# Performance work log

Measured on AMD Instinct MI355X. Metric: run time of the kernel, lower is better.

Reference implementation:

```python
import jax, jax.numpy as jnp
import numpy as np

B, C, H, W = 64, 512, 8, 8
K = 100            # num_class
H1, HID, L = 64, 128, 32   # ae_hidden[0], fixed hidd, ae_latent
CLIP = 100.0       # CSSRClassifier.clip_len
RED = -0.1         # model='pcssr' -> -1, times gamma=0.1
PUSH_THRESH = 10000.0


def setup_inputs() -> dict:
    key = jax.random.key(0)
    ks = jax.random.split(key, 9)
    s = lambda fan_in: 1.0 / np.sqrt(fan_in)  # kaiming-ish 1x1 conv init scale
    return {
        "x": jax.random.normal(ks[0], (B, C, H, W), jnp.float32),
        "ycls": jax.random.randint(ks[1], (B,), 0, K),
        "safe_margin_all": jax.random.normal(ks[2], (K,), jnp.float32),
        "safe_distance_all": jax.random.normal(ks[3], (K,), jnp.float32),
        "W1": jax.random.normal(ks[4], (K, H1, C), jnp.float32) * s(C),
        "W2": jax.random.normal(ks[5], (K, HID, H1), jnp.float32) * s(H1),
        "W3": jax.random.normal(ks[6], (K, L, HID), jnp.float32) * s(HID),
        "prototypes": jax.random.normal(ks[7], (K, L, H, W), jnp.float32),
        "prototypes1": jax.random.normal(ks[8], (K, L, H, W), jnp.float32),
    }


def reference(x, ycls, safe_margin_all, safe_distance_all, W1, W2, W3, prototypes, prototypes1):
    P = H * W
    xf = x.reshape(B, C, P)
    # per-class 1x1-conv encoder (tanh after every conv), batched over classes k
    h = jnp.tanh(jnp.einsum('koc,bcp->kbop', W1, xf))      # [K,B,H1,P]
    h = jnp.tanh(jnp.einsum('koi,kbip->kbop', W2, h))      # [K,B,HID,P]
    lt = jnp.tanh(jnp.einsum('koi,kbip->kbop', W3, h))     # [K,B,L,P]
    p = prototypes.reshape(K, 1, L, P)
    p1 = prototypes1.reshape(K, 1, L, P)
    # squared-L2 distance over channel dim, scaled by reduction, clipped
    er = jnp.clip(jnp.sum((lt - p) ** 2, axis=2) * RED, -CLIP, CLIP)    # [K,B,P]
    er1 = jnp.clip(jnp.sum((lt - p1) ** 2, axis=2) * RED, -CLIP, CLIP)  # [K,B,P]
    # training losses (pull on er1, push on er), vectorized across classes
    f = jnp.sum(er, axis=2)    # [K,B] spatial-summed errors
    f1 = jnp.sum(er1, axis=2)  # [K,B]
    cls_ids = jnp.arange(K)[:, None]
    mask_eq = (ycls[None, :] == cls_ids).astype(f.dtype)   # [K,B]
    n_eq = jnp.sum(mask_eq, axis=1)
    pull = jnp.sum(jnp.where(n_eq > 0,
                             jnp.sum(f1 * mask_eq, axis=1) / jnp.maximum(n_eq, 1.0),
                             0.0))
    comb = (1.0 - mask_eq) * (f < PUSH_THRESH).astype(f.dtype)
    n_comb = jnp.sum(comb, axis=1)
    push = jnp.sum(jnp.where(n_comb > 0,
                             jnp.sum(f * comb, axis=1) / jnp.maximum(n_comb, 1.0),
                             0.0))
    # cat per-class [B,1,H,W] errors along dim 1 -> [B,K,H,W]
    logits = jnp.transpose(er, (1, 0, 2)).reshape(B, K, H, W)
    logits1 = jnp.transpose(er1, (1, 0, 2)).reshape(B, K, H, W)
    return logits, logits1, pull, push
```

## Files before the change

kernel.cpp:

```cpp
#include <hip/hip_runtime.h>

typedef short  s16x8  __attribute__((ext_vector_type(8)));
typedef float  f32x16 __attribute__((ext_vector_type(16)));
typedef unsigned short u16;
typedef unsigned int   u32;
typedef unsigned long long u64b;

#define MFMA32(a,b,c) __builtin_amdgcn_mfma_f32_32x32x16_bf16((a),(b),(c),0,0,0)
#define KCLS 100
#define VMCNT(n) asm volatile("s_waitcnt vmcnt(" #n ")" ::: "memory")
#define BAR()    __builtin_amdgcn_s_barrier()

__device__ __forceinline__ u16 f2bf(float f) {
  return (u16)(__builtin_bit_cast(unsigned, f) >> 16);
}

__device__ __forceinline__ u32 pk2bf(float lo, float hi) {
#if __has_builtin(__builtin_amdgcn_perm)
  return __builtin_amdgcn_perm(__builtin_bit_cast(u32, hi),
                               __builtin_bit_cast(u32, lo), 0x07060302u);
#else
  return (__builtin_bit_cast(u32, lo) >> 16) | (__builtin_bit_cast(u32, hi) & 0xffff0000u);
#endif
}

__device__ __forceinline__ float tanh_fast(float x) {
  float e = __builtin_amdgcn_exp2f(x * 2.8853900817779268f);
  return 1.0f - 2.0f * __builtin_amdgcn_rcpf(e + 1.0f);
}

__device__ __forceinline__ void ld_lds16(const void* g, void* l) {
  __builtin_amdgcn_global_load_lds(
      (const __attribute__((address_space(1))) unsigned char*)g,
      (__attribute__((address_space(3))) unsigned char*)l, 16, 0, 0);
}

__global__ void prep(const float* __restrict__ x, const float* __restrict__ w1,
                     const float* __restrict__ w2, const float* __restrict__ w3,
                     u16* __restrict__ xF, u16* __restrict__ W1F,
                     u16* __restrict__ W2F, u16* __restrict__ W3F,
                     float* __restrict__ fz, float* __restrict__ out2) {
  __shared__ float tile[64][65];
  const int bid = blockIdx.x, t = threadIdx.x;
  if (bid == 0 && t < 2) out2[t] = 0.f;
  if (bid < 512) {
    const int b = bid >> 3, ck = bid & 7;
    #pragma unroll
    for (int j = 0; j < 4; j++) {
      int e4 = j * 1024 + t * 4;
      int c = e4 >> 6, p0 = e4 & 63;
      float4 v = *(const float4*)(x + ((size_t)b * 512 + ck * 64 + c) * 64 + p0);
      tile[c][p0] = v.x; tile[c][p0 + 1] = v.y; tile[c][p0 + 2] = v.z; tile[c][p0 + 3] = v.w;
    }
    __syncthreads();
    #pragma unroll
    for (int i = 0; i < 2; i++) {
      int s = i * 256 + t;
      int ksl = s >> 7, ph = (s >> 6) & 1, lane = s & 63;
      int cb = ksl * 16 + (lane >> 5) * 8, pp = ph * 32 + (lane & 31);
      u16 o[8];
      #pragma unroll
      for (int jj = 0; jj < 8; jj++) o[jj] = f2bf(tile[cb + jj][pp]);
      *(uint4*)(xF + (((size_t)b * 64 + (ck * 4 + ksl) * 2 + ph) * 512) + lane * 8) = *(uint4*)o;
    }
  } else if (bid < 1312) {
    const int wb = bid - 512, k = wb >> 3, ct = wb & 7;
    #pragma unroll
    for (int j = 0; j < 4; j++) {
      int e4 = j * 1024 + t * 4;
      int r = e4 >> 6, c = e4 & 63;
      float4 v = *(const float4*)(w1 + ((size_t)k * 64 + r) * 512 + ct * 64 + c);
      tile[r][c] = v.x; tile[r][c + 1] = v.y; tile[r][c + 2] = v.z; tile[r][c + 3] = v.w;
    }
    __syncthreads();
    #pragma unroll
    for (int i = 0; i < 2; i++) {
      int s = i * 256 + t;
      int frl = s >> 6, lane = s & 63;
      int m = (frl & 1) * 32 + (lane & 31);
      int cl = (frl >> 1) * 16 + (lane >> 5) * 8;
      u16 o[8];
      #pragma unroll
      for (int jj = 0; jj < 8; jj++) o[jj] = f2bf(tile[m][cl + jj]);
      *(uint4*)(W1F + ((size_t)(k * 64 + ct * 8 + frl) * 512) + lane * 8) = *(uint4*)o;
    }
  } else if (bid < 1512) {
    const int wb = bid - 1312, k = wb >> 1, mt = wb & 1;
    #pragma unroll
    for (int j = 0; j < 4; j++) {
      int e4 = j * 1024 + t * 4;
      int r = e4 >> 6, c = e4 & 63;
      float4 v = *(const float4*)(w2 + ((size_t)k * 128 + mt * 64 + r) * 64 + c);
      tile[r][c] = v.x; tile[r][c + 1] = v.y; tile[r][c + 2] = v.z; tile[r][c + 3] = v.w;
    }
    __syncthreads();
    #pragma unroll
    for (int i = 0; i < 2; i++) {
      int s = i * 256 + t;
      int frl = s >> 6, lane = s & 63;
      int kb = frl >> 1, m4l = frl & 1;
      int ml = m4l * 32 + (lane & 31);
      int cl = kb * 16 + (lane >> 5) * 8;
      u16 o[8];
      #pragma unroll
      for (int jj = 0; jj < 8; jj++) o[jj] = f2bf(tile[ml][cl + jj]);
      *(uint4*)(W2F + ((size_t)(k * 16 + kb * 4 + mt * 2 + m4l) * 512) + lane * 8) = *(uint4*)o;
    }
  } else if (bid < 1612) {
    const int k = bid - 1512;
    #pragma unroll
    for (int j = 0; j < 4; j++) {
      int e4 = j * 1024 + t * 4;
      int r = e4 >> 7, c = e4 & 127;
      float4 v = *(const float4*)(w3 + ((size_t)k * 32 + r) * 128 + c);
      int rr = r + ((c >> 6) << 5), cc = c & 63;
      tile[rr][cc] = v.x; tile[rr][cc + 1] = v.y; tile[rr][cc + 2] = v.z; tile[rr][cc + 3] = v.w;
    }
    __syncthreads();
    #pragma unroll
    for (int i = 0; i < 2; i++) {
      int s = i * 256 + t;
      int frl = s >> 6, lane = s & 63;
      int m = lane & 31;
      int c0 = frl * 16 + (lane >> 5) * 8;
      int rr = m + ((c0 >> 6) << 5), cc = c0 & 63;
      u16 o[8];
      #pragma unroll
      for (int jj = 0; jj < 8; jj++) o[jj] = f2bf(tile[rr][cc + jj]);
      *(uint4*)(W3F + ((size_t)(k * 8 + frl) * 512) + lane * 8) = *(uint4*)o;
    }
  } else {
    int i4 = (bid - 1612) * 256 + t;
    if (i4 < 3200) {
      float4 z = {0.f, 0.f, 0.f, 0.f};
      *(float4*)(fz + (size_t)i4 * 4) = z;
    }
  }
}

template<int GG>
__device__ __forceinline__ s16x8 mk_bfrag(const f32x16 a) {
  u32 P0 = pk2bf(tanh_fast(a[8 * GG + 0]), tanh_fast(a[8 * GG + 1]));
  u32 P1 = pk2bf(tanh_fast(a[8 * GG + 2]), tanh_fast(a[8 * GG + 3]));
  u32 Q0 = pk2bf(tanh_fast(a[8 * GG + 4]), tanh_fast(a[8 * GG + 5]));
  u32 Q1 = pk2bf(tanh_fast(a[8 * GG + 6]), tanh_fast(a[8 * GG + 7]));
  asm("v_permlane32_swap_b32 %0, %1" : "+v"(P0), "+v"(Q0));
  asm("v_permlane32_swap_b32 %0, %1" : "+v"(P1), "+v"(Q1));
  int4 wv = { (int)P0, (int)P1, (int)Q0, (int)Q1 };
  return __builtin_bit_cast(s16x8, wv);
}

__global__ __launch_bounds__(256, 4) void cssr_main(
    const u16* __restrict__ W1F, const u16* __restrict__ W2F, const u16* __restrict__ W3F,
    const u16* __restrict__ xF, const float* __restrict__ protos,
    const float* __restrict__ protos1, float* __restrict__ out,
    float* __restrict__ fw, float* __restrict__ f1w)
{
  __shared__ u16 pool[20480];
  const int bid = blockIdx.x;
  const int k = bid >> 5, bpair = bid & 31;
  const int tid = threadIdx.x, w = tid >> 6, lane = tid & 63;
  const int bq = w >> 1, ph = w & 1;
  const int b = bpair * 2 + bq;
  const int h = lane >> 5, nn = lane & 31;

  const u16* xw  = xF  + ((size_t)b * 64) * 512 + lane * 8;
  const u16* w1w = W1F + ((size_t)k * 64) * 512 + lane * 8;

  s16x8 Bc[4], Bn[4];
  #pragma unroll
  for (int ksl = 0; ksl < 4; ksl++)
    Bc[ksl] = *(const s16x8*)(xw + (ksl * 2 + ph) * 512);
  ld_lds16(w1w + (w * 2 + 0) * 512, &pool[(2 * w + 0) * 512]);
  ld_lds16(w1w + (w * 2 + 1) * 512, &pool[(2 * w + 1) * 512]);

  f32x16 acc1[2] = {};
  #pragma unroll
  for (int ci = 0; ci < 8; ci++) {
    const int cb = ci & 1;
    if (ci < 7) {
      #pragma unroll
      for (int ksl = 0; ksl < 4; ksl++)
        Bn[ksl] = *(const s16x8*)(xw + (((ci + 1) * 4 + ksl) * 2 + ph) * 512);
      ld_lds16(w1w + (((ci + 1) * 4 + w) * 2 + 0) * 512, &pool[(cb ^ 1) * 4096 + (2 * w + 0) * 512]);
      ld_lds16(w1w + (((ci + 1) * 4 + w) * 2 + 1) * 512, &pool[(cb ^ 1) * 4096 + (2 * w + 1) * 512]);
    } else {
      #pragma unroll
      for (int j = 0; j < 4; j++)
        ld_lds16(W2F + ((size_t)k * 16 + w * 4 + j) * 512 + lane * 8,
                 &pool[8192 + (w * 4 + j) * 512]);
      ld_lds16(W3F + ((size_t)k * 8 + w * 2 + 0) * 512 + lane * 8, &pool[16384 + (w * 2 + 0) * 512]);
      ld_lds16(W3F + ((size_t)k * 8 + w * 2 + 1) * 512 + lane * 8, &pool[16384 + (w * 2 + 1) * 512]);
    }
    VMCNT(6); BAR();
    __builtin_amdgcn_s_setprio(1);
    #pragma unroll
    for (int ksl = 0; ksl < 4; ksl++) {
      s16x8 A0 = *(const s16x8*)&pool[cb * 4096 + (ksl * 2 + 0) * 512 + lane * 8];
      s16x8 A1 = *(const s16x8*)&pool[cb * 4096 + (ksl * 2 + 1) * 512 + lane * 8];
      acc1[0] = MFMA32(A0, Bc[ksl], acc1[0]);
      acc1[1] = MFMA32(A1, Bc[ksl], acc1[1]);
    }
    __builtin_amdgcn_s_setprio(0);
    if (ci < 7) {
      #pragma unroll
      for (int ksl = 0; ksl < 4; ksl++) Bc[ksl] = Bn[ksl];
      BAR();
    }
  }

  s16x8 b1[4];
  b1[0] = mk_bfrag<0>(acc1[0]); b1[1] = mk_bfrag<1>(acc1[0]);
  b1[2] = mk_bfrag<0>(acc1[1]); b1[3] = mk_bfrag<1>(acc1[1]);

  VMCNT(2); BAR();

  f32x16 acc2[4] = {};
  __builtin_amdgcn_s_setprio(1);
  #pragma unroll
  for (int kb = 0; kb < 4; kb++) {
    #pragma unroll
    for (int m4 = 0; m4 < 4; m4++) {
      s16x8 A = *(const s16x8*)&pool[8192 + (kb * 4 + m4) * 512 + lane * 8];
      acc2[m4] = MFMA32(A, b1[kb], acc2[m4]);
    }
  }
  __builtin_amdgcn_s_setprio(0);

  VMCNT(0); BAR();

  const int p = ph * 32 + nn;
  const float* pr  = protos  + (size_t)k * 2048 + p;
  const float* pr1 = protos1 + (size_t)k * 2048 + p;
  float prv[16], pr1v[16];
  #pragma unroll
  for (int g = 0; g < 4; g++) {
    #pragma unroll
    for (int q = 0; q < 4; q++) {
      int m = q + 8 * g + 4 * h;
      prv [g * 4 + q] = pr [m * 64];
      pr1v[g * 4 + q] = pr1[m * 64];
    }
  }

  s16x8 b2[8];
  b2[0] = mk_bfrag<0>(acc2[0]); b2[1] = mk_bfrag<1>(acc2[0]);
  b2[2] = mk_bfrag<0>(acc2[1]); b2[3] = mk_bfrag<1>(acc2[1]);
  b2[4] = mk_bfrag<0>(acc2[2]); b2[5] = mk_bfrag<1>(acc2[2]);
  b2[6] = mk_bfrag<0>(acc2[3]); b2[7] = mk_bfrag<1>(acc2[3]);

  f32x16 acc3 = {};
  __builtin_amdgcn_s_setprio(1);
  #pragma unroll
  for (int kb = 0; kb < 8; kb++) {
    s16x8 A = *(const s16x8*)&pool[16384 + kb * 512 + lane * 8];
    acc3 = MFMA32(A, b2[kb], acc3);
  }
  __builtin_amdgcn_s_setprio(0);

  float d2 = 0.f, d21 = 0.f;
  #pragma unroll
  for (int g = 0; g < 4; g++) {
    #pragma unroll
    for (int q = 0; q < 4; q++) {
      float lt = tanh_fast(acc3[g * 4 + q]);
      float d = lt - prv [g * 4 + q];  d2  += d * d;
      float e = lt - pr1v[g * 4 + q];  d21 += e * e;
    }
  }
  d2 += __shfl_xor(d2, 32); d21 += __shfl_xor(d21, 32);
  float er  = fminf(fmaxf(d2  * -0.1f, -100.f), 100.f);
  float er1 = fminf(fmaxf(d21 * -0.1f, -100.f), 100.f);
  if (h == 0) {
    out[(size_t)b * 6400 + k * 64 + p]          = er;
    out[409600 + (size_t)b * 6400 + k * 64 + p] = er1;
  }
  float s = er, s1 = er1;
  s += __shfl_xor(s, 1);  s1 += __shfl_xor(s1, 1);
  s += __shfl_xor(s, 2);  s1 += __shfl_xor(s1, 2);
  s += __shfl_xor(s, 4);  s1 += __shfl_xor(s1, 4);
  s += __shfl_xor(s, 8);  s1 += __shfl_xor(s1, 8);
  s += __shfl_xor(s, 16); s1 += __shfl_xor(s1, 16);
  if (lane == 0) {
    atomicAdd(&fw [k * 64 + b], s);
    atomicAdd(&f1w[k * 64 + b], s1);
  }
}

__global__ void finalize(const float* __restrict__ f, const float* __restrict__ f1,
                         const int* __restrict__ ycls, float* __restrict__ out2) {
  const int k = blockIdx.x, b = threadIdx.x;
  float fv = f[k * 64 + b], f1v = f1[k * 64 + b];
  bool eq = (ycls[b] == k);
  bool cb = (!eq) && (fv < 10000.f);
  float s1 = eq ? f1v : 0.f, ne = eq ? 1.f : 0.f;
  float s  = cb ? fv  : 0.f, nc = cb ? 1.f : 0.f;
  #pragma unroll
  for (int o = 1; o < 64; o <<= 1) {
    s1 += __shfl_xor(s1, o); ne += __shfl_xor(ne, o);
    s  += __shfl_xor(s,  o); nc += __shfl_xor(nc, o);
  }
  if (b == 0) {
    if (ne > 0.f) atomicAdd(&out2[0], s1 / ne);
    if (nc > 0.f) atomicAdd(&out2[1], s / nc);
  }
}

extern "C" void kernel_launch(void* const* d_in, const int* in_sizes, int n_in,
                              void* d_out, int out_size, void* d_ws, size_t ws_size,
                              hipStream_t stream) {
  const float* x     = (const float*)d_in[0];
  const int*   ycls  = (const int*)d_in[1];
  const float* W1    = (const float*)d_in[4];
  const float* W2    = (const float*)d_in[5];
  const float* W3    = (const float*)d_in[6];
  const float* prot  = (const float*)d_in[7];
  const float* prot1 = (const float*)d_in[8];
  float* out = (float*)d_out;

  char* ws = (char*)d_ws;
  u16*  xFb = (u16*)(ws);
  u16*  W1F = (u16*)(ws + 4194304);
  u16*  W2F = (u16*)(ws + 10747904);
  u16*  W3F = (u16*)(ws + 12386304);
  float* fw  = (float*)(ws + 13205504);
  float* f1w = (float*)(ws + 13231104);

  prep<<<1625, 256, 0, stream>>>(x, W1, W2, W3, xFb, W1F, W2F, W3F,
                                 fw, out + 819200);
  cssr_main<<<KCLS * 32, 256, 0, stream>>>(W1F, W2F, W3F, xFb, prot, prot1,
                                           out, fw, f1w);
  finalize<<<KCLS, 64, 0, stream>>>(fw, f1w, ycls, out + 819200);
}
```

Baseline: 141.5 us.

## Fuse prep, main and finalize into one persistent cooperative kernel

Merges the three launches into a single cooperative kernel that runs the conversion phase, a grid sync, a dynamically scheduled main phase using an atomic work queue, another grid sync, and the loss finalisation. The goal is to remove launch gaps and tail effects between kernels. The cost is two grid-wide barriers, a per-unit atomic and block barrier for work fetching, and an occupancy query on every call. The grid is sized as occupancy times 256 CUs, and the original three-kernel path is kept as a fallback.

Result: slower. 327.3 us (+131.4%).

```diff
diff --git a/kernel.cpp b/kernel.cpp
--- a/kernel.cpp
+++ b/kernel.cpp
@@ -1,15 +1,19 @@
 #include <hip/hip_runtime.h>
+#include <hip/hip_cooperative_groups.h>
+
+namespace cg = cooperative_groups;
 
 typedef short  s16x8  __attribute__((ext_vector_type(8)));
 typedef float  f32x16 __attribute__((ext_vector_type(16)));
 typedef unsigned short u16;
 typedef unsigned int   u32;
-typedef unsigned long long u64b;
 
 #define MFMA32(a,b,c) __builtin_amdgcn_mfma_f32_32x32x16_bf16((a),(b),(c),0,0,0)
 #define KCLS 100
 #define VMCNT(n) asm volatile("s_waitcnt vmcnt(" #n ")" ::: "memory")
 #define BAR()    __builtin_amdgcn_s_barrier()
+
+__device__ int g_nextq;
 
 __device__ __forceinline__ u16 f2bf(float f) {
   return (u16)(__builtin_bit_cast(unsigned, f) >> 16);
@@ -33,109 +37,6 @@
   __builtin_amdgcn_global_load_lds(
       (const __attribute__((address_space(1))) unsigned char*)g,
       (__attribute__((address_space(3))) unsigned char*)l, 16, 0, 0);
-}
-
-__global__ void prep(const float* __restrict__ x, const float* __restrict__ w1,
-                     const float* __restrict__ w2, const float* __restrict__ w3,
-                     u16* __restrict__ xF, u16* __restrict__ W1F,
-                     u16* __restrict__ W2F, u16* __restrict__ W3F,
-                     float* __restrict__ fz, float* __restrict__ out2) {
-  __shared__ float tile[64][65];
-  const int bid = blockIdx.x, t = threadIdx.x;
-  if (bid == 0 && t < 2) out2[t] = 0.f;
-  if (bid < 512) {
-    const int b = bid >> 3, ck = bid & 7;
-    #pragma unroll
-    for (int j = 0; j < 4; j++) {
-      int e4 = j * 1024 + t * 4;
-      int c = e4 >> 6, p0 = e4 & 63;
-      float4 v = *(const float4*)(x + ((size_t)b * 512 + ck * 64 + c) * 64 + p0);
-      tile[c][p0] = v.x; tile[c][p0 + 1] = v.y; tile[c][p0 + 2] = v.z; tile[c][p0 + 3] = v.w;
-    }
-    __syncthreads();
-    #pragma unroll
-    for (int i = 0; i < 2; i++) {
-      int s = i * 256 + t;
-      int ksl = s >> 7, ph = (s >> 6) & 1, lane = s & 63;
-      int cb = ksl * 16 + (lane >> 5) * 8, pp = ph * 32 + (lane & 31);
-      u16 o[8];
-      #pragma unroll
-      for (int jj = 0; jj < 8; jj++) o[jj] = f2bf(tile[cb + jj][pp]);
-      *(uint4*)(xF + (((size_t)b * 64 + (ck * 4 + ksl) * 2 + ph) * 512) + lane * 8) = *(uint4*)o;
-    }
-  } else if (bid < 1312) {
-    const int wb = bid - 512, k = wb >> 3, ct = wb & 7;
-    #pragma unroll
-    for (int j = 0; j < 4; j++) {
-      int e4 = j * 1024 + t * 4;
-      int r = e4 >> 6, c = e4 & 63;
-      float4 v = *(const float4*)(w1 + ((size_t)k * 64 + r) * 512 + ct * 64 + c);
-      tile[r][c] = v.x; tile[r][c + 1] = v.y; tile[r][c + 2] = v.z; tile[r][c + 3] = v.w;
-    }
-    __syncthreads();
-    #pragma unroll
-    for (int i = 0; i < 2; i++) {
-      int s = i * 256 + t;
-      int frl = s >> 6, lane = s & 63;
-      int m = (frl & 1) * 32 + (lane & 31);
-      int cl = (frl >> 1) * 16 + (lane >> 5) * 8;
-      u16 o[8];
-      #pragma unroll
-      for (int jj = 0; jj < 8; jj++) o[jj] = f2bf(tile[m][cl + jj]);
-      *(uint4*)(W1F + ((size_t)(k * 64 + ct * 8 + frl) * 512) + lane * 8) = *(uint4*)o;
-    }
-  } else if (bid < 1512) {
-    const int wb = bid - 1312, k = wb >> 1, mt = wb & 1;
-    #pragma unroll
-    for (int j = 0; j < 4; j++) {
-      int e4 = j * 1024 + t * 4;
-      int r = e4 >> 6, c = e4 & 63;
-      float4 v = *(const float4*)(w2 + ((size_t)k * 128 + mt * 64 + r) * 64 + c);
-      tile[r][c] = v.x; tile[r][c + 1] = v.y; tile[r][c + 2] = v.z; tile[r][c + 3] = v.w;
-    }
-    __syncthreads();
-    #pragma unroll
-    for (int i = 0; i < 2; i++) {
-      int s = i * 256 + t;
-      int frl = s >> 6, lane = s & 63;
-      int kb = frl >> 1, m4l = frl & 1;
-      int ml = m4l * 32 + (lane & 31);
-      int cl = kb * 16 + (lane >> 5) * 8;
-      u16 o[8];
-      #pragma unroll
-      for (int jj = 0; jj < 8; jj++) o[jj] = f2bf(tile[ml][cl + jj]);
-      *(uint4*)(W2F + ((size_t)(k * 16 + kb * 4 + mt * 2 + m4l) * 512) + lane * 8) = *(uint4*)o;
-    }
-  } else if (bid < 1612) {
-    const int k = bid - 1512;
-    #pragma unroll
-    for (int j = 0; j < 4; j++) {
-      int e4 = j * 1024 + t * 4;
-      int r = e4 >> 7, c = e4 & 127;
-      float4 v = *(const float4*)(w3 + ((size_t)k * 32 + r) * 128 + c);
-      int rr = r + ((c >> 6) << 5), cc = c & 63;
-      tile[rr][cc] = v.x; tile[rr][cc + 1] = v.y; tile[rr][cc + 2] = v.z; tile[rr][cc + 3] = v.w;
-    }
-    __syncthreads();
-    #pragma unroll
-    for (int i = 0; i < 2; i++) {
-      int s = i * 256 + t;
-      int frl = s >> 6, lane = s & 63;
-      int m = lane & 31;
-      int c0 = frl * 16 + (lane >> 5) * 8;
-      int rr = m + ((c0 >> 6) << 5), cc = c0 & 63;
-      u16 o[8];
-      #pragma unroll
-      for (int jj = 0; jj < 8; jj++) o[jj] = f2bf(tile[rr][cc + jj]);
-      *(uint4*)(W3F + ((size_t)(k * 8 + frl) * 512) + lane * 8) = *(uint4*)o;
-    }
-  } else {
-    int i4 = (bid - 1612) * 256 + t;
-    if (i4 < 3200) {
-      float4 z = {0.f, 0.f, 0.f, 0.f};
-      *(float4*)(fz + (size_t)i4 * 4) = z;
-    }
-  }
 }
 
 template<int GG>
@@ -150,16 +51,115 @@
   return __builtin_bit_cast(s16x8, wv);
 }
 
-__global__ __launch_bounds__(256, 4) void cssr_main(
+__device__ __forceinline__ void prep_unit(
+    int au, int t, float (*tile)[65],
+    const float* __restrict__ x, const float* __restrict__ w1,
+    const float* __restrict__ w2, const float* __restrict__ w3,
+    u16* __restrict__ xF, u16* __restrict__ W1F,
+    u16* __restrict__ W2F, u16* __restrict__ W3F, float* __restrict__ fz) {
+  if (au < 512) {
+    const int b = au >> 3, ck = au & 7;
+    #pragma unroll
+    for (int j = 0; j < 4; j++) {
+      int e4 = j * 1024 + t * 4;
+      int c = e4 >> 6, p0 = e4 & 63;
+      float4 v = *(const float4*)(x + ((size_t)b * 512 + ck * 64 + c) * 64 + p0);
+      tile[c][p0] = v.x; tile[c][p0 + 1] = v.y; tile[c][p0 + 2] = v.z; tile[c][p0 + 3] = v.w;
+    }
+    __syncthreads();
+    #pragma unroll
+    for (int i = 0; i < 2; i++) {
+      int s = i * 256 + t;
+      int ksl = s >> 7, ph = (s >> 6) & 1, lane = s & 63;
+      int cb = ksl * 16 + (lane >> 5) * 8, pp = ph * 32 + (lane & 31);
+      u16 o[8];
+      #pragma unroll
+      for (int jj = 0; jj < 8; jj++) o[jj] = f2bf(tile[cb + jj][pp]);
+      *(uint4*)(xF + (((size_t)b * 64 + (ck * 4 + ksl) * 2 + ph) * 512) + lane * 8) = *(uint4*)o;
+    }
+  } else if (au < 1312) {
+    const int wb = au - 512, k = wb >> 3, ct = wb & 7;
+    #pragma unroll
+    for (int j = 0; j < 4; j++) {
+      int e4 = j * 1024 + t * 4;
+      int r = e4 >> 6, c = e4 & 63;
+      float4 v = *(const float4*)(w1 + ((size_t)k * 64 + r) * 512 + ct * 64 + c);
+      tile[r][c] = v.x; tile[r][c + 1] = v.y; tile[r][c + 2] = v.z; tile[r][c + 3] = v.w;
+    }
+    __syncthreads();
+    #pragma unroll
+    for (int i = 0; i < 2; i++) {
+      int s = i * 256 + t;
+      int frl = s >> 6, lane = s & 63;
+      int m = (frl & 1) * 32 + (lane & 31);
+      int cl = (frl >> 1) * 16 + (lane >> 5) * 8;
+      u16 o[8];
+      #pragma unroll
+      for (int jj = 0; jj < 8; jj++) o[jj] = f2bf(tile[m][cl + jj]);
+      *(uint4*)(W1F + ((size_t)(k * 64 + ct * 8 + frl) * 512) + lane * 8) = *(uint4*)o;
+    }
+  } else if (au < 1512) {
+    const int wb = au - 1312, k = wb >> 1, mt = wb & 1;
+    #pragma unroll
+    for (int j = 0; j < 4; j++) {
+      int e4 = j * 1024 + t * 4;
+      int r = e4 >> 6, c = e4 & 63;
+      float4 v = *(const float4*)(w2 + ((size_t)k * 128 + mt * 64 + r) * 64 + c);
+      tile[r][c] = v.x; tile[r][c + 1] = v.y; tile[r][c + 2] = v.z; tile[r][c + 3] = v.w;
+    }
+    __syncthreads();
+    #pragma unroll
+    for (int i = 0; i < 2; i++) {
+      int s = i * 256 + t;
+      int frl = s >> 6, lane = s & 63;
+      int kb = frl >> 1, m4l = frl & 1;
+      int ml = m4l * 32 + (lane & 31);
+      int cl = kb * 16 + (lane >> 5) * 8;
+      u16 o[8];
+      #pragma unroll
+      for (int jj = 0; jj < 8; jj++) o[jj] = f2bf(tile[ml][cl + jj]);
+      *(uint4*)(W2F + ((size_t)(k * 16 + kb * 4 + mt * 2 + m4l) * 512) + lane * 8) = *(uint4*)o;
+    }
+  } else if (au < 1612) {
+    const int k = au - 1512;
+    #pragma unroll
+    for (int j = 0; j < 4; j++) {
+      int e4 = j * 1024 + t * 4;
+      int r = e4 >> 7, c = e4 & 127;
+      float4 v = *(const float4*)(w3 + ((size_t)k * 32 + r) * 128 + c);
+      int rr = r + ((c >> 6) << 5), cc = c & 63;
+      tile[rr][cc] = v.x; tile[rr][cc + 1] = v.y; tile[rr][cc + 2] = v.z; tile[rr][cc + 3] = v.w;
+    }
+    __syncthreads();
+    #pragma unroll
+    for (int i = 0; i < 2; i++) {
+      int s = i * 256 + t;
+      int frl = s >> 6, lane = s & 63;
+      int m = lane & 31;
+      int c0 = frl * 16 + (lane >> 5) * 8;
+      int rr = m + ((c0 >> 6) << 5), cc = c0 & 63;
+      u16 o[8];
+      #pragma unroll
+      for (int jj = 0; jj < 8; jj++) o[jj] = f2bf(tile[rr][cc + jj]);
+      *(uint4*)(W3F + ((size_t)(k * 8 + frl) * 512) + lane * 8) = *(uint4*)o;
+    }
+  } else {
+    int i4 = (au - 1612) * 256 + t;
+    if (i4 < 3200) {
+      float4 z = {0.f, 0.f, 0.f, 0.f};
+      *(float4*)(fz + (size_t)i4 * 4) = z;
+    }
+  }
+}
+
+__device__ __forceinline__ void main_unit(
+    int u, int tid, u16* pool,
     const u16* __restrict__ W1F, const u16* __restrict__ W2F, const u16* __restrict__ W3F,
     const u16* __restrict__ xF, const float* __restrict__ protos,
     const float* __restrict__ protos1, float* __restrict__ out,
-    float* __restrict__ fw, float* __restrict__ f1w)
-{
-  __shared__ u16 pool[20480];
-  const int bid = blockIdx.x;
-  const int k = bid >> 5, bpair = bid & 31;
-  const int tid = threadIdx.x, w = tid >> 6, lane = tid & 63;
+    float* __restrict__ fw, float* __restrict__ f1w) {
+  const int k = u >> 5, bpair = u & 31;
+  const int w = tid >> 6, lane = tid & 63;
   const int bq = w >> 1, ph = w & 1;
   const int b = bpair * 2 + bq;
   const int h = lane >> 5, nn = lane & 31;
@@ -285,6 +285,83 @@
     atomicAdd(&fw [k * 64 + b], s);
     atomicAdd(&f1w[k * 64 + b], s1);
   }
+}
+
+__global__ __launch_bounds__(256, 4) void cssr_all(
+    const float* __restrict__ x, const float* __restrict__ w1,
+    const float* __restrict__ w2, const float* __restrict__ w3,
+    const int* __restrict__ ycls,
+    const float* __restrict__ protos, const float* __restrict__ protos1,
+    u16* __restrict__ xF, u16* __restrict__ W1F,
+    u16* __restrict__ W2F, u16* __restrict__ W3F,
+    float* __restrict__ fw, float* __restrict__ f1w,
+    float* __restrict__ out, float* __restrict__ out2)
+{
+  __shared__ __align__(16) char smem[40960];
+  const int bid = blockIdx.x, t = threadIdx.x;
+
+  {
+    float (*tile)[65] = reinterpret_cast<float(*)[65]>(smem);
+    if (bid == 0 && t == 0) { out2[0] = 0.f; out2[1] = 0.f; g_nextq = 0; }
+    for (int au = bid; au < 1625; au += gridDim.x) {
+      prep_unit(au, t, tile, x, w1, w2, w3, xF, W1F, W2F, W3F, fw);
+      __syncthreads();
+    }
+  }
+  cg::this_grid().sync();
+
+  {
+    u16* pool = (u16*)smem;
+    volatile int* uslot = (volatile int*)(smem + 32768);
+    for (;;) {
+      BAR();
+      if (t == 0) *uslot = atomicAdd(&g_nextq, 1);
+      __syncthreads();
+      const int u = *uslot;
+      if (u >= 3200) break;
+      main_unit(u, t, pool, W1F, W2F, W3F, xF, protos, protos1, out, fw, f1w);
+    }
+  }
+  cg::this_grid().sync();
+
+  if (bid < KCLS && t < 64) {
+    const int k = bid, b = t;
+    float fv = fw[k * 64 + b], f1v = f1w[k * 64 + b];
+    bool eq = (ycls[b] == k);
+    bool cb = (!eq) && (fv < 10000.f);
+    float s1 = eq ? f1v : 0.f, ne = eq ? 1.f : 0.f;
+    float s  = cb ? fv  : 0.f, nc = cb ? 1.f : 0.f;
+    #pragma unroll
+    for (int o = 1; o < 64; o <<= 1) {
+      s1 += __shfl_xor(s1, o); ne += __shfl_xor(ne, o);
+      s  += __shfl_xor(s,  o); nc += __shfl_xor(nc, o);
+    }
+    if (b == 0) {
+      if (ne > 0.f) atomicAdd(&out2[0], s1 / ne);
+      if (nc > 0.f) atomicAdd(&out2[1], s / nc);
+    }
+  }
+}
+
+__global__ void prep(const float* __restrict__ x, const float* __restrict__ w1,
+                     const float* __restrict__ w2, const float* __restrict__ w3,
+                     u16* __restrict__ xF, u16* __restrict__ W1F,
+                     u16* __restrict__ W2F, u16* __restrict__ W3F,
+                     float* __restrict__ fz, float* __restrict__ out2) {
+  __shared__ float tile[64][65];
+  const int bid = blockIdx.x, t = threadIdx.x;
+  if (bid == 0 && t < 2) out2[t] = 0.f;
+  prep_unit(bid, t, tile, x, w1, w2, w3, xF, W1F, W2F, W3F, fz);
+}
+
+__global__ __launch_bounds__(256, 4) void cssr_main(
+    const u16* __restrict__ W1F, const u16* __restrict__ W2F, const u16* __restrict__ W3F,
+    const u16* __restrict__ xF, const float* __restrict__ protos,
+    const float* __restrict__ protos1, float* __restrict__ out,
+    float* __restrict__ fw, float* __restrict__ f1w)
+{
+  __shared__ u16 pool[20480];
+  main_unit(blockIdx.x, threadIdx.x, pool, W1F, W2F, W3F, xF, protos, protos1, out, fw, f1w);
 }
 
 __global__ void finalize(const float* __restrict__ f, const float* __restrict__ f1,
@@ -320,15 +397,31 @@
 
   char* ws = (char*)d_ws;
   u16*  xFb = (u16*)(ws);
-  u16*  W1F = (u16*)(ws + 4194304);
-  u16*  W2F = (u16*)(ws + 10747904);
-  u16*  W3F = (u16*)(ws + 12386304);
+  u16*  W1Fp = (u16*)(ws + 4194304);
+  u16*  W2Fp = (u16*)(ws + 10747904);
+  u16*  W3Fp = (u16*)(ws + 12386304);
   float* fw  = (float*)(ws + 13205504);
   float* f1w = (float*)(ws + 13231104);
-
-  prep<<<1625, 256, 0, stream>>>(x, W1, W2, W3, xFb, W1F, W2F, W3F,
-                                 fw, out + 819200);
-  cssr_main<<<KCLS * 32, 256, 0, stream>>>(W1F, W2F, W3F, xFb, prot, prot1,
-                                           out, fw, f1w);
-  finalize<<<KCLS, 64, 0, stream>>>(fw, f1w, ycls, out + 819200);
-}
+  float* out2 = out + 819200;
+
+  bool coop_done = false;
+  int occ = 0;
+  if (hipOccupancyMaxActiveBlocksPerMultiprocessor(&occ, cssr_all, 256, 0) == hipSuccess
+      && occ >= 1) {
+    int nblk = occ * 256;
+    if (nblk > 3200) nblk = 3200;
+    void* args[] = { (void*)&x, (void*)&W1, (void*)&W2, (void*)&W3, (void*)&ycls,
+                     (void*)&prot, (void*)&prot1,
+                     (void*)&xFb, (void*)&W1Fp, (void*)&W2Fp, (void*)&W3Fp,
+                     (void*)&fw, (void*)&f1w, (void*)&out, (void*)&out2 };
+    hipError_t e = hipLaunchCooperativeKernel(cssr_all, dim3(nblk), dim3(256),
+                                              args, 0, stream);
+    coop_done = (e == hipSuccess);
+  }
+  if (!coop_done) {
+    prep<<<1625, 256, 0, stream>>>(x, W1, W2, W3, xFb, W1Fp, W2Fp, W3Fp, fw, out2);
+    cssr_main<<<KCLS * 32, 256, 0, stream>>>(W1Fp, W2Fp, W3Fp, xFb, prot, prot1,
+                                             out, fw, f1w);
+    finalize<<<KCLS, 64, 0, stream>>>(fw, f1w, ycls, out2);
+  }
+}
```
